# Kernel optimization log

Measured on AMD Instinct MI355X. Metric: run time of the kernel, lower is better.

The kernel has to match this reference:

```python
import jax, jax.numpy as jnp
import numpy as np

N_NODES = 100000
N_EDGES = 1000000
EMB = 64
HID = 64
N_CLASSES = 1
LEAKY_SLOPE = 0.01  # flax.linen.leaky_relu default


def setup_inputs() -> dict:
    key = jax.random.key(0)
    k1, k2, k3, k4, k5 = jax.random.split(key, 5)
    node_ids = jnp.arange(N_NODES, dtype=jnp.int32)
    senders = jax.random.randint(k1, (N_EDGES,), 0, N_NODES, dtype=jnp.int32)
    receivers = jax.random.randint(k2, (N_EDGES,), 0, N_NODES, dtype=jnp.int32)
    embed_table = jax.random.normal(k3, (N_NODES, EMB), dtype=jnp.float32) * 0.05
    W1 = jax.random.normal(k4, (EMB, HID), dtype=jnp.float32) * (1.0 / np.sqrt(EMB))
    W2 = jax.random.normal(k5, (HID, N_CLASSES), dtype=jnp.float32) * (1.0 / np.sqrt(HID))
    b2 = jnp.zeros((N_CLASSES,), dtype=jnp.float32)
    return {"node_ids": node_ids, "senders": senders, "receivers": receivers,
            "embed_table": embed_table, "W1": W1, "W2": W2, "b2": b2}


def gcn_aggregate(x, senders, receivers, n_nodes, symmetric):
    # Faithful to jraph.GraphConvolution: update_node_fn is applied BEFORE this.
    if symmetric:
        ones = jnp.ones_like(senders, dtype=x.dtype)
        send_deg = jax.ops.segment_sum(ones, senders, num_segments=n_nodes)
        recv_deg = jax.ops.segment_sum(ones, receivers, num_segments=n_nodes)
        x = x * jax.lax.rsqrt(jnp.maximum(send_deg, 1.0))[:, None]
        x = jax.ops.segment_sum(x[senders], receivers, num_segments=n_nodes)  # [N, d]
        x = x * jax.lax.rsqrt(jnp.maximum(recv_deg, 1.0))[:, None]
    else:
        x = jax.ops.segment_sum(x[senders], receivers, num_segments=n_nodes)
    return x


def reference(node_ids, senders, receivers, embed_table, W1, W2, b2):
    n = node_ids.shape[0]
    # GraphMapFeatures(embed_node_fn=nn.Embed(...))
    x = embed_table[node_ids]                      # [N, EMB]
    # GraphConvolution(Dense(hidden, use_bias=False), symmetric_normalization=True)
    x = x @ W1                                     # [N, HID]
    x = gcn_aggregate(x, senders, receivers, n, symmetric=True)
    x = jax.nn.leaky_relu(x, negative_slope=LEAKY_SLOPE)
    # GraphConvolution(Dense(classes), symmetric_normalization=False)
    x = x @ W2 + b2                                # [N, C]
    x = gcn_aggregate(x, senders, receivers, n, symmetric=False)
    return jax.nn.sigmoid(x)
```

## Files before the change

kernel.cpp:

```cpp
#include <hip/hip_runtime.h>
#include <hip/hip_bf16.h>

#define N_NODES 100000
#define N_EDGES 1000000
#define SCAN_B 256
#define N_BLOCKS_SCAN ((N_NODES + SCAN_B - 1) / SCAN_B)
#define H_BLOCKS 1024

#define RANGES 4
#define RSIZE  25000
#define RWORDS 12500
#define CHUNKS 32
#define CHUNK_EDGES (N_EDGES / CHUNKS)
#define HRSIZE  12500
#define HRWORDS 6250


__device__ __forceinline__ unsigned f32_to_bf16(float v) {
    unsigned u = __float_as_uint(v);
    return (u + 0x7fffu + ((u >> 16) & 1u)) >> 16;
}

__global__ void k_hist(const int* __restrict__ senders,
                       const int* __restrict__ receivers,
                       unsigned* __restrict__ ghist_s,
                       unsigned* __restrict__ ghist_r) {
    __shared__ unsigned lds[RWORDS];
    int blk = blockIdx.x;
    int arr = blk >> 7;
    int rem = blk & 127;
    int r   = rem >> 5;
    int c   = rem & 31;
    const int* __restrict__ src = arr ? receivers : senders;
    unsigned* __restrict__ gh   = arr ? ghist_r : ghist_s;
    int t = threadIdx.x;

    for (int w = t; w < RWORDS; w += 1024) lds[w] = 0u;
    __syncthreads();

    int base = r * RSIZE;
    int beg  = c * CHUNK_EDGES;
    int end  = beg + CHUNK_EDGES;
    for (int i = beg + t; i < end; i += 1024) {
        unsigned idx = (unsigned)(src[i] - base);
        if (idx < (unsigned)RSIZE)
            atomicAdd(&lds[idx >> 1], 1u << ((idx & 1) * 16));
    }
    __syncthreads();

    unsigned* __restrict__ dst = gh + (size_t)rem * RWORDS;
    for (int w = t; w < RWORDS; w += 1024) dst[w] = lds[w];
}

__global__ void k_scanA2(const unsigned* __restrict__ ghist_s,
                         const unsigned* __restrict__ ghist_r,
                         int* __restrict__ cnt_r, float* __restrict__ rs,
                         int* __restrict__ blockSums) {
    __shared__ int s[SCAN_B];
    int t = threadIdx.x;
    int idx = blockIdx.x * SCAN_B + t;
    int v = 0;
    if (idx < N_NODES) {
        int r = idx / RSIZE;
        int bin = idx - r * RSIZE;
        int w = bin >> 1, sh = (bin & 1) * 16;
        const unsigned* __restrict__ gr = ghist_r + (size_t)(r * CHUNKS) * RWORDS + w;
        const unsigned* __restrict__ gs = ghist_s + (size_t)(r * CHUNKS) * RWORDS + w;
        unsigned sr_ = 0, ss_ = 0;
#pragma unroll
        for (int c = 0; c < CHUNKS; ++c) {
            sr_ += (gr[(size_t)c * RWORDS] >> sh) & 0xffffu;
            ss_ += (gs[(size_t)c * RWORDS] >> sh) & 0xffffu;
        }
        v = (int)sr_;
        cnt_r[idx] = v;
        rs[idx] = rsqrtf(fmaxf((float)ss_, 1.0f));
    }
    s[t] = v;
    __syncthreads();
    for (int off = 1; off < SCAN_B; off <<= 1) {
        int x = (t >= off) ? s[t - off] : 0;
        __syncthreads();
        s[t] += x;
        __syncthreads();
    }
    if (t == SCAN_B - 1) blockSums[blockIdx.x] = s[t];
}

__global__ void k_scanCD_h(const int* __restrict__ cnt_r,
                           const int* __restrict__ blockSums,
                           const unsigned* __restrict__ ghist_r,
                           int* __restrict__ row_start,
                           int* __restrict__ coff,
                           const float* __restrict__ emb,
                           const float* __restrict__ rs,
                           const float* __restrict__ W1,
                           unsigned short* __restrict__ h16) {
    __shared__ int s[SCAN_B];
    int t = threadIdx.x;
    int b = blockIdx.x;

    if (b < N_BLOCKS_SCAN) {
        int acc = 0;
        for (int j = t; j < b; j += SCAN_B) acc += blockSums[j];
        s[t] = acc;
        __syncthreads();
        for (int off = SCAN_B / 2; off > 0; off >>= 1) {
            if (t < off) s[t] += s[t + off];
            __syncthreads();
        }
        int blockOff = s[0];
        __syncthreads();

        int idx = b * SCAN_B + t;
        int v = (idx < N_NODES) ? cnt_r[idx] : 0;
        s[t] = v;
        __syncthreads();
        for (int off = 1; off < SCAN_B; off <<= 1) {
            int x = (t >= off) ? s[t - off] : 0;
            __syncthreads();
            s[t] += x;
            __syncthreads();
        }
        if (idx < N_NODES) {
            int run = blockOff + s[t] - v;
            row_start[idx] = run;
            int r = idx / RSIZE;
            int bin = idx - r * RSIZE;
            int w = bin >> 1, sh = (bin & 1) * 16;
            const unsigned* __restrict__ gr = ghist_r + (size_t)(r * CHUNKS) * RWORDS + w;
            int* __restrict__ co = coff + (size_t)(r * CHUNKS) * RSIZE + bin;
#pragma unroll
            for (int c = 0; c < CHUNKS; ++c) {
                co[(size_t)c * RSIZE] = run;
                run += (int)((gr[(size_t)c * RWORDS] >> sh) & 0xffffu);
            }
        }
        if (b == 0 && t == 0) row_start[N_NODES] = N_EDGES;
    } else {
        int lane = t & 63;
        int wib  = t >> 6;
        int gw   = (b - N_BLOCKS_SCAN) * 4 + wib;
        const int nw = H_BLOCKS * 4;

        float w1c[64];
#pragma unroll
        for (int k = 0; k < 64; ++k) w1c[k] = W1[k * 64 + lane];

        for (int n = gw; n < N_NODES; n += nw) {
            float e = emb[(size_t)n * 64 + lane] * rs[n];
            float a = 0.f;
            int ei = __float_as_int(e);
#pragma unroll
            for (int k = 0; k < 64; ++k)
                a += __int_as_float(__builtin_amdgcn_readlane(ei, k)) * w1c[k];
            h16[(size_t)n * 64 + lane] = (unsigned short)f32_to_bf16(a);
        }
    }
}

__global__ void k_fill2(const int* __restrict__ senders,
                        const int* __restrict__ receivers,
                        const int* __restrict__ coff,
                        int* __restrict__ col) {
    __shared__ unsigned lds[HRWORDS];
    int r8 = blockIdx.x >> 5;
    int c  = blockIdx.x & 31;
    int sr = r8 >> 1, hs = r8 & 1;
    int t  = threadIdx.x;

    for (int w = t; w < HRWORDS; w += 1024) lds[w] = 0u;
    __syncthreads();

    int base = r8 * HRSIZE;
    int beg  = c * CHUNK_EDGES, end = beg + CHUNK_EDGES;
    const int* __restrict__ co =
        coff + (size_t)(sr * CHUNKS + c) * RSIZE + hs * HRSIZE;
    for (int i = beg + t; i < end; i += 1024) {
        unsigned idx = (unsigned)(receivers[i] - base);
        if (idx < (unsigned)HRSIZE) {
            int sh = (idx & 1) * 16;
            unsigned old = atomicAdd(&lds[idx >> 1], 1u << sh);
            int rank = (int)((old >> sh) & 0xffffu);
            col[co[idx] + rank] = senders[i];
        }
    }
}

__global__ void k_agg_post(const int* __restrict__ row_start,
                           const int* __restrict__ col,
                           const unsigned* __restrict__ h32,
                           const float* __restrict__ W2,
                           const float* __restrict__ b2,
                           float* __restrict__ z) {
    int gtid = blockIdx.x * blockDim.x + threadIdx.x;
    int wid  = gtid >> 6;
    int lane = threadIdx.x & 63;
    int half = lane >> 5;
    int hl   = lane & 31;
    int n = wid * 2 + half;
    if (n >= N_NODES) return;

    int start = row_start[n];
    int end   = row_start[n + 1];
    float a0 = 0.f, a1 = 0.f;
    int i = start;
    for (; i + 3 < end; i += 4) {
        int s0 = col[i], s1 = col[i + 1], s2 = col[i + 2], s3 = col[i + 3];
        unsigned u0 = h32[(size_t)s0 * 32 + hl];
        unsigned u1 = h32[(size_t)s1 * 32 + hl];
        unsigned u2 = h32[(size_t)s2 * 32 + hl];
        unsigned u3 = h32[(size_t)s3 * 32 + hl];
        a0 += (__uint_as_float(u0 << 16) + __uint_as_float(u1 << 16)) +
              (__uint_as_float(u2 << 16) + __uint_as_float(u3 << 16));
        a1 += (__uint_as_float(u0 & 0xffff0000u) + __uint_as_float(u1 & 0xffff0000u)) +
              (__uint_as_float(u2 & 0xffff0000u) + __uint_as_float(u3 & 0xffff0000u));
    }
    for (; i < end; ++i) {
        unsigned u = h32[(size_t)col[i] * 32 + hl];
        a0 += __uint_as_float(u << 16);
        a1 += __uint_as_float(u & 0xffff0000u);
    }

    float rsq = rsqrtf(fmaxf((float)(end - start), 1.0f));
    float x0 = a0 * rsq, x1 = a1 * rsq;
    x0 = (x0 > 0.f) ? x0 : 0.01f * x0;
    x1 = (x1 > 0.f) ? x1 : 0.01f * x1;
    float2 w2 = ((const float2*)W2)[hl];
    float p = x0 * w2.x + x1 * w2.y;
#pragma unroll
    for (int off = 16; off > 0; off >>= 1) p += __shfl_xor(p, off, 64);
    if (hl == 0) z[n] = p + b2[0];
}

__global__ void k_agg2_sigmoid(const int* __restrict__ row_start,
                               const int* __restrict__ col,
                               const float* __restrict__ z,
                               float* __restrict__ out) {
    int n = blockIdx.x * blockDim.x + threadIdx.x;
    if (n >= N_NODES) return;
    int start = row_start[n];
    int end   = row_start[n + 1];
    float acc = 0.f;
    int i = start;
    for (; i + 3 < end; i += 4) {
        float a = z[col[i]],     b = z[col[i + 1]];
        float c = z[col[i + 2]], d = z[col[i + 3]];
        acc += (a + b) + (c + d);
    }
    for (; i < end; ++i) acc += z[col[i]];
    out[n] = 1.0f / (1.0f + expf(-acc));
}

extern "C" void kernel_launch(void* const* d_in, const int* in_sizes, int n_in,
                              void* d_out, int out_size, void* d_ws, size_t ws_size,
                              hipStream_t stream) {
    const int* senders    = (const int*)d_in[1];
    const int* receivers  = (const int*)d_in[2];
    const float* emb      = (const float*)d_in[3];
    const float* W1       = (const float*)d_in[4];
    const float* W2       = (const float*)d_in[5];
    const float* b2       = (const float*)d_in[6];
    float* out            = (float*)d_out;

    char* ws = (char*)d_ws;
    unsigned*       ghist_s   = (unsigned*)(ws);
    unsigned*       ghist_r   = (unsigned*)(ws + 6400000);
    int*            coff      = (int*)(ws + 12800000);
    int*            cnt_r     = (int*)(ws + 25600000);
    int*            row_start = (int*)(ws + 26000000);
    int*            blockSums = (int*)(ws + 26400016);
    float*          rs        = (float*)(ws + 26403200);
    int*            col       = (int*)(ws + 26803200);
    unsigned short* h16       = (unsigned short*)(ws + 30803200);
    float*          z         = (float*)(ws + 43603200);

    const int B = 256;
    k_hist<<<2 * RANGES * CHUNKS, 1024, 0, stream>>>(senders, receivers, ghist_s, ghist_r);
    k_scanA2<<<N_BLOCKS_SCAN, SCAN_B, 0, stream>>>(ghist_s, ghist_r, cnt_r, rs, blockSums);
    k_scanCD_h<<<N_BLOCKS_SCAN + H_BLOCKS, B, 0, stream>>>(
        cnt_r, blockSums, ghist_r, row_start, coff, emb, rs, W1, h16);
    k_fill2<<<RANGES * CHUNKS * 2, 1024, 0, stream>>>(senders, receivers, coff, col);
    k_agg_post<<<12500, B, 0, stream>>>(row_start, col, (const unsigned*)h16, W2, b2, z);
    k_agg2_sigmoid<<<(N_NODES + B - 1) / B, B, 0, stream>>>(row_start, col, z, out);
}
```

Measured before the change: 213.3 us.

## Replace LDS-chunked histogram CSR build with global atomics and per-edge ranks

Drops the multi-pass LDS histogram over range/chunk tiles and the per-chunk offset table. Degrees now come from global atomicAdd over edges, with the returned old count kept as a 16-bit rank per edge. A later fill pass scatters each sender to row_start plus its rank. This removes repeated full edge scans and a large coff/ghist workspace, at the cost of contended global atomics and a non-deterministic column order within each row.

```diff
diff --git a/kernel.cpp b/kernel.cpp
--- a/kernel.cpp
+++ b/kernel.cpp
@@ -7,74 +7,50 @@
 #define N_BLOCKS_SCAN ((N_NODES + SCAN_B - 1) / SCAN_B)
 #define H_BLOCKS 1024
 
-#define RANGES 4
-#define RSIZE  25000
-#define RWORDS 12500
-#define CHUNKS 32
-#define CHUNK_EDGES (N_EDGES / CHUNKS)
-#define HRSIZE  12500
-#define HRWORDS 6250
-
 
 __device__ __forceinline__ unsigned f32_to_bf16(float v) {
     unsigned u = __float_as_uint(v);
     return (u + 0x7fffu + ((u >> 16) & 1u)) >> 16;
 }
 
-__global__ void k_hist(const int* __restrict__ senders,
-                       const int* __restrict__ receivers,
-                       unsigned* __restrict__ ghist_s,
-                       unsigned* __restrict__ ghist_r) {
-    __shared__ unsigned lds[RWORDS];
-    int blk = blockIdx.x;
-    int arr = blk >> 7;
-    int rem = blk & 127;
-    int r   = rem >> 5;
-    int c   = rem & 31;
-    const int* __restrict__ src = arr ? receivers : senders;
-    unsigned* __restrict__ gh   = arr ? ghist_r : ghist_s;
-    int t = threadIdx.x;
-
-    for (int w = t; w < RWORDS; w += 1024) lds[w] = 0u;
-    __syncthreads();
-
-    int base = r * RSIZE;
-    int beg  = c * CHUNK_EDGES;
-    int end  = beg + CHUNK_EDGES;
-    for (int i = beg + t; i < end; i += 1024) {
-        unsigned idx = (unsigned)(src[i] - base);
-        if (idx < (unsigned)RSIZE)
-            atomicAdd(&lds[idx >> 1], 1u << ((idx & 1) * 16));
-    }
-    __syncthreads();
-
-    unsigned* __restrict__ dst = gh + (size_t)rem * RWORDS;
-    for (int w = t; w < RWORDS; w += 1024) dst[w] = lds[w];
-}
-
-__global__ void k_scanA2(const unsigned* __restrict__ ghist_s,
-                         const unsigned* __restrict__ ghist_r,
-                         int* __restrict__ cnt_r, float* __restrict__ rs,
-                         int* __restrict__ blockSums) {
+__global__ void k_zero(uint4* __restrict__ p) {
+    int i = blockIdx.x * blockDim.x + threadIdx.x;
+    if (i < 50000) p[i] = make_uint4(0u, 0u, 0u, 0u);
+}
+
+__global__ void k_deg_rank(const int4* __restrict__ s4,
+                           const int4* __restrict__ r4,
+                           int* __restrict__ send_deg,
+                           int* __restrict__ cnt_r,
+                           unsigned short* __restrict__ rank16) {
+    int i = blockIdx.x * blockDim.x + threadIdx.x;
+    if (i >= N_EDGES / 4) return;
+    int4 s = s4[i];
+    int4 r = r4[i];
+    atomicAdd(&send_deg[s.x], 1);
+    atomicAdd(&send_deg[s.y], 1);
+    atomicAdd(&send_deg[s.z], 1);
+    atomicAdd(&send_deg[s.w], 1);
+    unsigned k0 = (unsigned)atomicAdd(&cnt_r[r.x], 1);
+    unsigned k1 = (unsigned)atomicAdd(&cnt_r[r.y], 1);
+    unsigned k2 = (unsigned)atomicAdd(&cnt_r[r.z], 1);
+    unsigned k3 = (unsigned)atomicAdd(&cnt_r[r.w], 1);
+    uint2 packed = make_uint2((k0 & 0xffffu) | (k1 << 16),
+                              (k2 & 0xffffu) | (k3 << 16));
+    *(uint2*)(rank16 + 4 * (size_t)i) = packed;
+}
+
+__global__ void k_scanA(const int* __restrict__ cnt_r,
+                        const int* __restrict__ send_deg,
+                        float* __restrict__ rs,
+                        int* __restrict__ blockSums) {
     __shared__ int s[SCAN_B];
     int t = threadIdx.x;
     int idx = blockIdx.x * SCAN_B + t;
     int v = 0;
     if (idx < N_NODES) {
-        int r = idx / RSIZE;
-        int bin = idx - r * RSIZE;
-        int w = bin >> 1, sh = (bin & 1) * 16;
-        const unsigned* __restrict__ gr = ghist_r + (size_t)(r * CHUNKS) * RWORDS + w;
-        const unsigned* __restrict__ gs = ghist_s + (size_t)(r * CHUNKS) * RWORDS + w;
-        unsigned sr_ = 0, ss_ = 0;
-#pragma unroll
-        for (int c = 0; c < CHUNKS; ++c) {
-            sr_ += (gr[(size_t)c * RWORDS] >> sh) & 0xffffu;
-            ss_ += (gs[(size_t)c * RWORDS] >> sh) & 0xffffu;
-        }
-        v = (int)sr_;
-        cnt_r[idx] = v;
-        rs[idx] = rsqrtf(fmaxf((float)ss_, 1.0f));
+        v = cnt_r[idx];
+        rs[idx] = rsqrtf(fmaxf((float)send_deg[idx], 1.0f));
     }
     s[t] = v;
     __syncthreads();
@@ -89,9 +65,7 @@
 
 __global__ void k_scanCD_h(const int* __restrict__ cnt_r,
                            const int* __restrict__ blockSums,
-                           const unsigned* __restrict__ ghist_r,
                            int* __restrict__ row_start,
-                           int* __restrict__ coff,
                            const float* __restrict__ emb,
                            const float* __restrict__ rs,
                            const float* __restrict__ W1,
@@ -122,20 +96,7 @@
             s[t] += x;
             __syncthreads();
         }
-        if (idx < N_NODES) {
-            int run = blockOff + s[t] - v;
-            row_start[idx] = run;
-            int r = idx / RSIZE;
-            int bin = idx - r * RSIZE;
-            int w = bin >> 1, sh = (bin & 1) * 16;
-            const unsigned* __restrict__ gr = ghist_r + (size_t)(r * CHUNKS) * RWORDS + w;
-            int* __restrict__ co = coff + (size_t)(r * CHUNKS) * RSIZE + bin;
-#pragma unroll
-            for (int c = 0; c < CHUNKS; ++c) {
-                co[(size_t)c * RSIZE] = run;
-                run += (int)((gr[(size_t)c * RWORDS] >> sh) & 0xffffu);
-            }
-        }
+        if (idx < N_NODES) row_start[idx] = blockOff + s[t] - v;
         if (b == 0 && t == 0) row_start[N_NODES] = N_EDGES;
     } else {
         int lane = t & 63;
@@ -159,32 +120,20 @@
     }
 }
 
-__global__ void k_fill2(const int* __restrict__ senders,
-                        const int* __restrict__ receivers,
-                        const int* __restrict__ coff,
-                        int* __restrict__ col) {
-    __shared__ unsigned lds[HRWORDS];
-    int r8 = blockIdx.x >> 5;
-    int c  = blockIdx.x & 31;
-    int sr = r8 >> 1, hs = r8 & 1;
-    int t  = threadIdx.x;
-
-    for (int w = t; w < HRWORDS; w += 1024) lds[w] = 0u;
-    __syncthreads();
-
-    int base = r8 * HRSIZE;
-    int beg  = c * CHUNK_EDGES, end = beg + CHUNK_EDGES;
-    const int* __restrict__ co =
-        coff + (size_t)(sr * CHUNKS + c) * RSIZE + hs * HRSIZE;
-    for (int i = beg + t; i < end; i += 1024) {
-        unsigned idx = (unsigned)(receivers[i] - base);
-        if (idx < (unsigned)HRSIZE) {
-            int sh = (idx & 1) * 16;
-            unsigned old = atomicAdd(&lds[idx >> 1], 1u << sh);
-            int rank = (int)((old >> sh) & 0xffffu);
-            col[co[idx] + rank] = senders[i];
-        }
-    }
+__global__ void k_fill(const int4* __restrict__ s4,
+                       const int4* __restrict__ r4,
+                       const uint2* __restrict__ rk2,
+                       const int* __restrict__ row_start,
+                       int* __restrict__ col) {
+    int i = blockIdx.x * blockDim.x + threadIdx.x;
+    if (i >= N_EDGES / 4) return;
+    int4 s = s4[i];
+    int4 r = r4[i];
+    uint2 rk = rk2[i];
+    col[row_start[r.x] + (int)(rk.x & 0xffffu)] = s.x;
+    col[row_start[r.y] + (int)(rk.x >> 16)]     = s.y;
+    col[row_start[r.z] + (int)(rk.y & 0xffffu)] = s.z;
+    col[row_start[r.w] + (int)(rk.y >> 16)]     = s.w;
 }
 
 __global__ void k_agg_post(const int* __restrict__ row_start,
@@ -264,23 +213,27 @@
     float* out            = (float*)d_out;
 
     char* ws = (char*)d_ws;
-    unsigned*       ghist_s   = (unsigned*)(ws);
-    unsigned*       ghist_r   = (unsigned*)(ws + 6400000);
-    int*            coff      = (int*)(ws + 12800000);
-    int*            cnt_r     = (int*)(ws + 25600000);
-    int*            row_start = (int*)(ws + 26000000);
-    int*            blockSums = (int*)(ws + 26400016);
-    float*          rs        = (float*)(ws + 26403200);
-    int*            col       = (int*)(ws + 26803200);
-    unsigned short* h16       = (unsigned short*)(ws + 30803200);
-    float*          z         = (float*)(ws + 43603200);
+    int*            cnt_r     = (int*)(ws);
+    int*            send_deg  = (int*)(ws + 400000);
+    int*            row_start = (int*)(ws + 800000);
+    int*            blockSums = (int*)(ws + 1200016);
+    float*          rs        = (float*)(ws + 1201600);
+    unsigned short* rank16    = (unsigned short*)(ws + 1601600);
+    int*            col       = (int*)(ws + 3601600);
+    unsigned short* h16       = (unsigned short*)(ws + 7601664);
+    float*          z         = (float*)(ws + 20401664);
 
     const int B = 256;
-    k_hist<<<2 * RANGES * CHUNKS, 1024, 0, stream>>>(senders, receivers, ghist_s, ghist_r);
-    k_scanA2<<<N_BLOCKS_SCAN, SCAN_B, 0, stream>>>(ghist_s, ghist_r, cnt_r, rs, blockSums);
+    const int QBLK = (N_EDGES / 4 + B - 1) / B;
+
+    k_zero<<<196, B, 0, stream>>>((uint4*)ws);
+    k_deg_rank<<<QBLK, B, 0, stream>>>((const int4*)senders, (const int4*)receivers,
+                                       send_deg, cnt_r, rank16);
+    k_scanA<<<N_BLOCKS_SCAN, SCAN_B, 0, stream>>>(cnt_r, send_deg, rs, blockSums);
     k_scanCD_h<<<N_BLOCKS_SCAN + H_BLOCKS, B, 0, stream>>>(
-        cnt_r, blockSums, ghist_r, row_start, coff, emb, rs, W1, h16);
-    k_fill2<<<RANGES * CHUNKS * 2, 1024, 0, stream>>>(senders, receivers, coff, col);
+        cnt_r, blockSums, row_start, emb, rs, W1, h16);
+    k_fill<<<QBLK, B, 0, stream>>>((const int4*)senders, (const int4*)receivers,
+                                   (const uint2*)rank16, row_start, col);
     k_agg_post<<<12500, B, 0, stream>>>(row_start, col, (const unsigned*)h16, W2, b2, z);
     k_agg2_sigmoid<<<(N_NODES + B - 1) / B, B, 0, stream>>>(row_start, col, z, out);
 }
```

Measured after the change: 263.9 us. 23.7% more time.
